# Performance work log

Measured on AMD Instinct MI355X. Metric: run time of the kernel, lower is better.

The kernel has to match this reference:

```python
import math
import jax, jax.numpy as jnp
import numpy as np

B, S, D, H = 4, 2048, 768, 12
HD = D // H  # 64


def setup_inputs() -> dict:
    key = jax.random.key(0)
    ks = jax.random.split(key, 10)
    sc = 0.02
    return {
        "hidden_states": jax.random.normal(ks[0], (B, S, D), dtype=jnp.float32),
        "attention_mask": jax.random.randint(ks[1], (1, H, S, S), 0, 2).astype(jnp.bool_),
        "q_w": jax.random.normal(ks[2], (D, D), dtype=jnp.float32) * sc,
        "q_b": jax.random.normal(ks[3], (D,), dtype=jnp.float32) * sc,
        "k_w": jax.random.normal(ks[4], (D, D), dtype=jnp.float32) * sc,
        "k_b": jax.random.normal(ks[5], (D,), dtype=jnp.float32) * sc,
        "v_w": jax.random.normal(ks[6], (D, D), dtype=jnp.float32) * sc,
        "v_b": jax.random.normal(ks[7], (D,), dtype=jnp.float32) * sc,
        "out_w": jax.random.normal(ks[8], (D, D), dtype=jnp.float32) * sc,
        "out_b": jax.random.normal(ks[9], (D,), dtype=jnp.float32) * sc,
    }


def _split_heads(x):
    # [B, S, D] -> [B, H, S, HD]
    b, s, _ = x.shape
    return x.reshape(b, s, H, HD).transpose(0, 2, 1, 3)


def reference(hidden_states, attention_mask, q_w, q_b, k_w, k_b, v_w, v_b, out_w, out_b):
    q = _split_heads(hidden_states @ q_w.T + q_b)
    k = _split_heads(hidden_states @ k_w.T + k_b)
    v = _split_heads(hidden_states @ v_w.T + v_b)
    scores = jnp.einsum("bhqd,bhkd->bhqk", q, k) / math.sqrt(HD)
    # prune_mode, before softmax: masked_fill(~mask, -inf)
    scores = jnp.where(attention_mask, scores, -jnp.inf)
    probs = jax.nn.softmax(scores, axis=-1)  # [B, H, S, S]
    ctx = jnp.einsum("bhqk,bhkd->bhqd", probs, v)
    ctx = ctx.transpose(0, 2, 1, 3).reshape(hidden_states.shape[0], -1, D)
    return ctx @ out_w.T + out_b
```

## Files before the change

### kernel.cpp

```cpp
#include <hip/hip_runtime.h>
#include <hip/hip_bf16.h>

#define B_ 4
#define S_ 2048
#define D_ 768
#define H_ 12
#define HD_ 64

typedef __attribute__((ext_vector_type(8))) short bf16x8;
typedef __attribute__((ext_vector_type(4))) float floatx4;

#define QSCALE 0.18033688011112042f

__device__ __forceinline__ unsigned short f2bf(float x) {
    union { float f; unsigned int u; } v; v.f = x;
    unsigned int r = v.u + 0x7fffu + ((v.u >> 16) & 1u);
    return (unsigned short)(r >> 16);
}

__device__ __forceinline__ unsigned int pk2bf(float a, float b) {
    __hip_bfloat162 h = __float22bfloat162_rn(make_float2(a, b));
    unsigned int u;
    __builtin_memcpy(&u, &h, 4);
    return u;
}

__device__ __forceinline__ void gload_lds16(const void* g, void* l) {
    __builtin_amdgcn_global_load_lds(
        (const __attribute__((address_space(1))) unsigned int*)g,
        (__attribute__((address_space(3))) unsigned int*)l, 16, 0, 0);
}

__device__ __forceinline__ bf16x8 ld_b64x2(const unsigned short* p) {
    union { bf16x8 v; unsigned long long q[2]; } u;
    u.q[0] = *(const unsigned long long*)p;
    u.q[1] = *(const unsigned long long*)(p + 4);
    return u.v;
}

__global__ void prep(const float* __restrict__ hs,
                     const float* __restrict__ w0, const float* __restrict__ w1,
                     const float* __restrict__ w2, const float* __restrict__ w3,
                     const int* __restrict__ mask,
                     unsigned short* __restrict__ Xb,
                     unsigned short* __restrict__ Wb,
                     unsigned long long* __restrict__ bits) {
    int bid = blockIdx.x;
    int t = threadIdx.x;
    if (bid < 6144) {
        int i = bid * 256 + t;
        float4 f = ((const float4*)hs)[i];
        ushort4 o;
        o.x = f2bf(f.x); o.y = f2bf(f.y); o.z = f2bf(f.z); o.w = f2bf(f.w);
        ((ushort4*)Xb)[i] = o;
    } else if (bid < 8448) {
        int q = bid - 6144;
        int wid = q / 576;
        const float* src = (wid == 0) ? w0 : (wid == 1) ? w1 : (wid == 2) ? w2 : w3;
        unsigned short* d = Wb + (size_t)wid * 589824;
        int i = (q - wid * 576) * 256 + t;
        float4 f = ((const float4*)src)[i];
        ushort4 o;
        o.x = f2bf(f.x); o.y = f2bf(f.y); o.z = f2bf(f.z); o.w = f2bf(f.w);
        ((ushort4*)d)[i] = o;
    } else {
        size_t gw = ((size_t)(bid - 8448) * 256 + t) >> 6;
        int lane = t & 63;
        size_t base = gw * 256;
        unsigned long long b0 = __ballot(mask[base + lane] != 0);
        unsigned long long b1 = __ballot(mask[base + 64 + lane] != 0);
        unsigned long long b2 = __ballot(mask[base + 128 + lane] != 0);
        unsigned long long b3 = __ballot(mask[base + 192 + lane] != 0);
        if (lane == 0) {
            bits[gw * 4 + 0] = b0; bits[gw * 4 + 1] = b1;
            bits[gw * 4 + 2] = b2; bits[gw * 4 + 3] = b3;
        }
    }
}

__global__ __launch_bounds__(256) void qkv_gemm(
    const unsigned short* __restrict__ Xb,
    const unsigned short* __restrict__ Wq, const unsigned short* __restrict__ Wk,
    const unsigned short* __restrict__ Wv,
    const float* __restrict__ bq, const float* __restrict__ bk,
    const float* __restrict__ bv,
    unsigned short* __restrict__ Qo, unsigned short* __restrict__ Ko,
    unsigned short* __restrict__ Vo)
{
    const int z = blockIdx.z;
    const unsigned short* W = (z == 0) ? Wq : (z == 1) ? Wk : Wv;
    const float* bias = (z == 0) ? bq : (z == 1) ? bk : bv;
    unsigned short* Out = (z == 0) ? Qo : (z == 1) ? Ko : Vo;
    const float scale = (z == 0) ? QSCALE : 1.0f;

    const int m0 = blockIdx.x * 128;
    const int n0 = blockIdx.y * 128;

    __shared__ alignas(16) unsigned short SMall[16384];
    unsigned short* SM = SMall;

    const int t = threadIdx.x;
    const int lane = t & 63, w = t >> 6;
    const int c = lane & 15, quad = lane >> 4;
    const int wm = (w & 1) * 64, wn = (w >> 1) * 64;

    const int srowq = lane >> 2, sc8 = (lane & 3) * 8;

    floatx4 acc[4][4];
#pragma unroll
    for (int i = 0; i < 4; i++)
#pragma unroll
        for (int j = 0; j < 4; j++) acc[i][j] = (floatx4){0.f, 0.f, 0.f, 0.f};

#pragma unroll
    for (int i = 0; i < 2; i++) {
        int chunk = i * 4 + w;
        int row = chunk * 16 + srowq;
        gload_lds16(&Xb[(size_t)(m0 + row) * 768 + sc8], &SMall[chunk * 512]);
        gload_lds16(&W [(size_t)(n0 + row) * 768 + sc8], &SMall[4096 + chunk * 512]);
    }

    for (int it = 0; it < 24; it++) {
        const int cur = it & 1;
        __syncthreads();
        if (it + 1 < 24) {
            int k1 = (it + 1) * 32;
#pragma unroll
            for (int i = 0; i < 2; i++) {
                int chunk = i * 4 + w;
                int row = chunk * 16 + srowq;
                gload_lds16(&Xb[(size_t)(m0 + row) * 768 + k1 + sc8],
                            &SMall[(cur ^ 1) * 8192 + chunk * 512]);
                gload_lds16(&W [(size_t)(n0 + row) * 768 + k1 + sc8],
                            &SMall[(cur ^ 1) * 8192 + 4096 + chunk * 512]);
            }
        }
        const unsigned short* As = &SMall[cur * 8192];
        const unsigned short* Bs = As + 4096;
        bf16x8 a[4], b[4];
#pragma unroll
        for (int i = 0; i < 4; i++)
            a[i] = *(const bf16x8*)&As[(wm + i * 16 + c) * 32 + quad * 8];
#pragma unroll
        for (int j = 0; j < 4; j++)
            b[j] = *(const bf16x8*)&Bs[(wn + j * 16 + c) * 32 + quad * 8];
#pragma unroll
        for (int i = 0; i < 4; i++)
#pragma unroll
            for (int j = 0; j < 4; j++)
                acc[i][j] = __builtin_amdgcn_mfma_f32_16x16x32_bf16(
                    a[i], b[j], acc[i][j], 0, 0, 0);
    }
    __syncthreads();

    const int bb = m0 >> 11, ssb = m0 & 2047;
    if (z == 2) {
#pragma unroll
        for (int half = 0; half < 2; half++) {
            if ((w >> 1) == half) {
#pragma unroll
                for (int j = 0; j < 4; j++) {
                    int n_l = j * 16 + c;
                    float bias_n = bias[n0 + half * 64 + n_l];
#pragma unroll
                    for (int i = 0; i < 4; i++) {
#pragma unroll
                        for (int r = 0; r < 4; r++) {
                            int m = wm + i * 16 + quad * 4 + r;
                            int ms = m ^ (c << 3);
                            SM[n_l * 128 + ms] = f2bf(acc[i][j][r] + bias_n);
                        }
                    }
                }
            }
            __syncthreads();
#pragma unroll
            for (int rb = 0; rb < 2; rb++) {
                int n_l = (t >> 3) + rb * 32;
                int ch = t & 7;
                int n_abs = n0 + half * 64 + n_l;
                int hh = n_abs >> 6, dd = n_abs & 63;
                unsigned short* dst =
                    Out + (((size_t)(bb * H_ + hh)) * 64 + dd) * S_ + ssb;
#pragma unroll
                for (int p = 0; p < 2; p++) {
                    int mc = ch + p * 8;
                    uint4 v = *(const uint4*)&SM[n_l * 128 + ((mc ^ (n_l & 15)) * 8)];
                    *(uint4*)&dst[mc * 8] = v;
                }
            }
            __syncthreads();
        }
    } else {
#pragma unroll
        for (int half = 0; half < 2; half++) {
            if ((w >> 1) == half) {
#pragma unroll
                for (int j = 0; j < 4; j++) {
                    float bias_n = bias[n0 + half * 64 + j * 16 + c];
#pragma unroll
                    for (int i = 0; i < 4; i++) {
#pragma unroll
                        for (int r = 0; r < 4; r++) {
                            int m = wm + i * 16 + quad * 4 + r;
                            int chunk = (j * 2 + (c >> 3)) ^ ((m >> 1) & 7);
                            SM[m * 64 + chunk * 8 + (c & 7)] =
                                f2bf((acc[i][j][r] + bias_n) * scale);
                        }
                    }
                }
            }
            __syncthreads();
            {
                int hh = (n0 >> 6) + half;
                unsigned short* dst =
                    Out + ((size_t)(bb * H_ + hh) * S_ + ssb) * 64;
#pragma unroll
                for (int i = 0; i < 4; i++) {
                    int idx = i * 256 + t;
                    int m = idx >> 3, ch = idx & 7;
                    uint4 v = *(const uint4*)&SM[m * 64 + ((ch ^ ((m >> 1) & 7)) * 8)];
                    *(uint4*)&dst[(size_t)m * 64 + ch * 8] = v;
                }
            }
            __syncthreads();
        }
    }
}

__global__ __launch_bounds__(256) void out_gemm(
    const unsigned short* __restrict__ Cb, const unsigned short* __restrict__ Wo,
    const float* __restrict__ bo, float* __restrict__ out)
{
    const int m0 = blockIdx.x * 64;
    const int n0 = blockIdx.y * 128;

    __shared__ alignas(16) unsigned short SMall[12288];

    const int t = threadIdx.x;
    const int lane = t & 63, w = t >> 6;
    const int c = lane & 15, quad = lane >> 4;
    const int wm = (w & 1) * 32, wn = (w >> 1) * 64;

    const int arow = w * 16 + (lane >> 2);
    const int brow0 = (lane >> 2);
    const int sc8 = (lane & 3) * 8;

    floatx4 acc[2][4];
#pragma unroll
    for (int i = 0; i < 2; i++)
#pragma unroll
        for (int j = 0; j < 4; j++) acc[i][j] = (floatx4){0.f, 0.f, 0.f, 0.f};

    gload_lds16(&Cb[(size_t)(m0 + arow) * 768 + sc8], &SMall[w * 512]);
#pragma unroll
    for (int i = 0; i < 2; i++) {
        int chunk = i * 4 + w;
        gload_lds16(&Wo[(size_t)(n0 + chunk * 16 + brow0) * 768 + sc8],
                    &SMall[2048 + chunk * 512]);
    }

    for (int it = 0; it < 24; it++) {
        const int cur = it & 1;
        __syncthreads();
        if (it + 1 < 24) {
            int k1 = (it + 1) * 32;
            gload_lds16(&Cb[(size_t)(m0 + arow) * 768 + k1 + sc8],
                        &SMall[(cur ^ 1) * 6144 + w * 512]);
#pragma unroll
            for (int i = 0; i < 2; i++) {
                int chunk = i * 4 + w;
                gload_lds16(&Wo[(size_t)(n0 + chunk * 16 + brow0) * 768 + k1 + sc8],
                            &SMall[(cur ^ 1) * 6144 + 2048 + chunk * 512]);
            }
        }
        const unsigned short* As = &SMall[cur * 6144];
        const unsigned short* Bs = As + 2048;
        bf16x8 a[2], b[4];
#pragma unroll
        for (int i = 0; i < 2; i++)
            a[i] = *(const bf16x8*)&As[(wm + i * 16 + c) * 32 + quad * 8];
#pragma unroll
        for (int j = 0; j < 4; j++)
            b[j] = *(const bf16x8*)&Bs[(wn + j * 16 + c) * 32 + quad * 8];
#pragma unroll
        for (int i = 0; i < 2; i++)
#pragma unroll
            for (int j = 0; j < 4; j++)
                acc[i][j] = __builtin_amdgcn_mfma_f32_16x16x32_bf16(
                    a[i], b[j], acc[i][j], 0, 0, 0);
    }
    __syncthreads();

    float* SMf = (float*)SMall;
#pragma unroll
    for (int qtr = 0; qtr < 4; qtr++) {
        if ((w >> 1) == (qtr >> 1)) {
#pragma unroll
            for (int jj = 0; jj < 2; jj++) {
                int j = (qtr & 1) * 2 + jj;
                float bias_n = bo[n0 + wn + j * 16 + c];
                int chunk = jj * 4 + (c >> 2);
#pragma unroll
                for (int i = 0; i < 2; i++) {
#pragma unroll
                    for (int r = 0; r < 4; r++) {
                        int m = wm + i * 16 + quad * 4 + r;
                        SMf[m * 32 + ((chunk ^ (m & 7)) * 4) + (c & 3)] =
                            acc[i][j][r] + bias_n;
                    }
                }
            }
        }
        __syncthreads();
#pragma unroll
        for (int i = 0; i < 2; i++) {
            int idx = i * 256 + t;
            int m = idx >> 3, ch = idx & 7;
            float4 v = *(const float4*)&SMf[m * 32 + ((ch ^ (m & 7)) * 4)];
            *(float4*)&out[(size_t)(m0 + m) * 768 + n0 + qtr * 32 + ch * 4] = v;
        }
        __syncthreads();
    }
}

__global__ __launch_bounds__(256) void attn(
    const unsigned short* __restrict__ Q, const unsigned short* __restrict__ K,
    const unsigned short* __restrict__ Vt,
    const unsigned long long* __restrict__ mbits,
    unsigned short* __restrict__ ctx)
{
    const int qt = blockIdx.x;
    const int bh = blockIdx.y;
    const int b = bh / H_, h = bh % H_;

    const unsigned short* Qp = Q + (size_t)bh * S_ * 64 + (size_t)qt * 128 * 64;
    const unsigned short* Kp = K + (size_t)bh * S_ * 64;
    const unsigned short* Vp = Vt + (size_t)bh * 64 * S_;

    __shared__ alignas(16) unsigned short Ks[2][64 * 64];
    __shared__ alignas(16) unsigned short Vs[2][64 * 64];
    __shared__ alignas(16) unsigned short Ps[4][2][16 * 68];

    const int t = threadIdx.x;
    const int lane = t & 63, w = t >> 6;
    const int c = lane & 15, quad = lane >> 4;

    bf16x8 aq[2][2];
#pragma unroll
    for (int st = 0; st < 2; st++) {
        aq[st][0] = *(const bf16x8*)&Qp[(size_t)(w * 32 + st * 16 + c) * 64 + quad * 8];
        aq[st][1] = *(const bf16x8*)&Qp[(size_t)(w * 32 + st * 16 + c) * 64 + 32 + quad * 8];
    }

    const unsigned long long* mrow =
        mbits + ((size_t)h * S_ + qt * 128 + w * 32 + quad * 4) * (S_ / 64);

    floatx4 acc_o[2][4];
#pragma unroll
    for (int st = 0; st < 2; st++)
#pragma unroll
        for (int i = 0; i < 4; i++) acc_o[st][i] = (floatx4){0.f, 0.f, 0.f, 0.f};
    float lp[2][4] = {{0.f, 0.f, 0.f, 0.f}, {0.f, 0.f, 0.f, 0.f}};

    const int srow = (lane >> 3);
    const int rc0 = ((quad     ) ^ (c & 7)) * 8;
    const int rc1 = ((quad + 4) ^ (c & 7)) * 8;

#pragma unroll
    for (int i = 0; i < 2; i++) {
        int chunk = i * 4 + w;
        int row = chunk * 8 + srow;
        int col8 = (((lane & 7) ^ ((row >> 2) & 7))) * 8;
        gload_lds16(&Kp[(size_t)row * 64 + col8], &Ks[0][chunk * 512]);
        gload_lds16(&Vp[(size_t)row * S_ + col8], &Vs[0][chunk * 512]);
    }

    for (int kt = 0; kt < S_ / 64; kt++) {
        const int cur = kt & 1;
        __syncthreads();
        if (kt + 1 < S_ / 64) {
#pragma unroll
            for (int i = 0; i < 2; i++) {
                int chunk = i * 4 + w;
                int row = chunk * 8 + srow;
                int col8 = (((lane & 7) ^ ((row >> 2) & 7))) * 8;
                gload_lds16(&Kp[(size_t)((kt + 1) * 64 + row) * 64 + col8],
                            &Ks[cur ^ 1][chunk * 512]);
                gload_lds16(&Vp[(size_t)row * S_ + (kt + 1) * 64 + col8],
                            &Vs[cur ^ 1][chunk * 512]);
            }
        }

        floatx4 sacc[2][4];
        __builtin_amdgcn_s_setprio(1);
#pragma unroll
        for (int nt = 0; nt < 4; nt++) {
            int kr = 4 * c + nt;
            bf16x8 bk0 = *(const bf16x8*)&Ks[cur][kr * 64 + rc0];
            bf16x8 bk1 = *(const bf16x8*)&Ks[cur][kr * 64 + rc1];
#pragma unroll
            for (int st = 0; st < 2; st++) {
                floatx4 zz = (floatx4){0.f, 0.f, 0.f, 0.f};
                zz = __builtin_amdgcn_mfma_f32_16x16x32_bf16(aq[st][0], bk0, zz, 0, 0, 0);
                zz = __builtin_amdgcn_mfma_f32_16x16x32_bf16(aq[st][1], bk1, zz, 0, 0, 0);
                sacc[st][nt] = zz;
            }
        }
        __builtin_amdgcn_s_setprio(0);

        asm volatile("" ::: "memory");
#pragma unroll
        for (int st = 0; st < 2; st++) {
#pragma unroll
            for (int r = 0; r < 4; r++) {
                unsigned int nib =
                    (unsigned int)(mrow[st * 16 * (S_ / 64) + r * (S_ / 64) + kt] >> (4 * c)) & 15u;
                float p0 = (nib & 1u) ? __builtin_amdgcn_exp2f(sacc[st][0][r]) : 0.f;
                float p1 = (nib & 2u) ? __builtin_amdgcn_exp2f(sacc[st][1][r]) : 0.f;
                float p2 = (nib & 4u) ? __builtin_amdgcn_exp2f(sacc[st][2][r]) : 0.f;
                float p3 = (nib & 8u) ? __builtin_amdgcn_exp2f(sacc[st][3][r]) : 0.f;
                lp[st][r] += (p0 + p1) + (p2 + p3);
                unsigned long long pk =
                    (unsigned long long)pk2bf(p0, p1) |
                    ((unsigned long long)pk2bf(p2, p3) << 32);
                *(unsigned long long*)&Ps[w][st][(quad * 4 + r) * 68 + 4 * c] = pk;
            }
        }
        asm volatile("" ::: "memory");

        bf16x8 ap[2][2];
#pragma unroll
        for (int st = 0; st < 2; st++) {
            ap[st][0] = ld_b64x2(&Ps[w][st][c * 68 + quad * 8]);
            ap[st][1] = ld_b64x2(&Ps[w][st][c * 68 + 32 + quad * 8]);
        }

        __builtin_amdgcn_s_setprio(1);
#pragma unroll
        for (int nt = 0; nt < 4; nt++) {
            int vr = 4 * c + nt;
            bf16x8 bv0 = *(const bf16x8*)&Vs[cur][vr * 64 + rc0];
            bf16x8 bv1 = *(const bf16x8*)&Vs[cur][vr * 64 + rc1];
#pragma unroll
            for (int st = 0; st < 2; st++) {
                acc_o[st][nt] = __builtin_amdgcn_mfma_f32_16x16x32_bf16(ap[st][0], bv0, acc_o[st][nt], 0, 0, 0);
                acc_o[st][nt] = __builtin_amdgcn_mfma_f32_16x16x32_bf16(ap[st][1], bv1, acc_o[st][nt], 0, 0, 0);
            }
        }
        __builtin_amdgcn_s_setprio(0);
    }

#pragma unroll
    for (int st = 0; st < 2; st++)
#pragma unroll
        for (int r = 0; r < 4; r++) {
            float s = lp[st][r];
#pragma unroll
            for (int o = 1; o < 16; o <<= 1) s += __shfl_xor(s, o, 64);
            lp[st][r] = s;
        }

#pragma unroll
    for (int st = 0; st < 2; st++)
#pragma unroll
        for (int nt = 0; nt < 4; nt++)
#pragma unroll
            for (int r = 0; r < 4; r++) {
                int qrow = qt * 128 + w * 32 + st * 16 + quad * 4 + r;
                int dd = 4 * c + nt;
                float v = acc_o[st][nt][r] / lp[st][r];
                ctx[((size_t)b * S_ + qrow) * 768 + h * 64 + dd] = f2bf(v);
            }
}

extern "C" void kernel_launch(void* const* d_in, const int* in_sizes, int n_in,
                              void* d_out, int out_size, void* d_ws, size_t ws_size,
                              hipStream_t stream) {
    const float* hs    = (const float*)d_in[0];
    const int*   mask  = (const int*)d_in[1];
    const float* q_w   = (const float*)d_in[2];
    const float* q_b   = (const float*)d_in[3];
    const float* k_w   = (const float*)d_in[4];
    const float* k_b   = (const float*)d_in[5];
    const float* v_w   = (const float*)d_in[6];
    const float* v_b   = (const float*)d_in[7];
    const float* out_w = (const float*)d_in[8];
    const float* out_b = (const float*)d_in[9];
    float* out = (float*)d_out;

    unsigned short* Xb  = (unsigned short*)d_ws;
    unsigned short* Wqb = Xb + 6291456;
    unsigned short* Wkb = Wqb + 589824;
    unsigned short* Wvb = Wkb + 589824;
    unsigned short* Wob = Wvb + 589824;
    unsigned short* Qb  = Wob + 589824;
    unsigned short* Kb  = Qb + 6291456;
    unsigned short* Vtb = Kb + 6291456;
    unsigned short* Cb  = Vtb + 6291456;
    unsigned long long* mbits = (unsigned long long*)(Cb + 6291456);

    prep<<<57600, 256, 0, stream>>>(hs, q_w, k_w, v_w, out_w, mask, Xb, Wqb, mbits);
    qkv_gemm<<<dim3(64, 6, 3), 256, 0, stream>>>(Xb, Wqb, Wkb, Wvb,
                                                 q_b, k_b, v_b, Qb, Kb, Vtb);
    attn<<<dim3(16, 48), 256, 0, stream>>>(Qb, Kb, Vtb, mbits, Cb);
    out_gemm<<<dim3(128, 6), 256, 0, stream>>>(Cb, Wob, out_b, out);
}
```

Before: 497.0 us.

## Coarsen mask-pack blocks, remap block order per XCD, split QK softmax into halves

The mask-packing part of prep now has each block handle eight wave-groups instead of one, which cuts the prep grid from 57600 to 14592 blocks. The qkv_gemm, out_gemm and attn kernels remap their linear block IDs with an interleave of 8, so that neighbouring tiles that share operands land on the same XCD and its L2. The attention inner loop is split into two halves, so the exp/mask/pack work of one half can overlap with the MFMAs of the other, and the s_setprio hints are removed. These changes are meant to lower launch and scheduling overhead, improve cache locality, and hide softmax latency behind matrix ops, at the cost of smaller 4-byte LDS stores and a different instruction schedule.

```diff
diff --git a/kernel.cpp b/kernel.cpp
--- a/kernel.cpp
+++ b/kernel.cpp
@@ -64,16 +64,20 @@
         o.x = f2bf(f.x); o.y = f2bf(f.y); o.z = f2bf(f.z); o.w = f2bf(f.w);
         ((ushort4*)d)[i] = o;
     } else {
-        size_t gw = ((size_t)(bid - 8448) * 256 + t) >> 6;
-        int lane = t & 63;
-        size_t base = gw * 256;
-        unsigned long long b0 = __ballot(mask[base + lane] != 0);
-        unsigned long long b1 = __ballot(mask[base + 64 + lane] != 0);
-        unsigned long long b2 = __ballot(mask[base + 128 + lane] != 0);
-        unsigned long long b3 = __ballot(mask[base + 192 + lane] != 0);
-        if (lane == 0) {
-            bits[gw * 4 + 0] = b0; bits[gw * 4 + 1] = b1;
-            bits[gw * 4 + 2] = b2; bits[gw * 4 + 3] = b3;
+        int q = bid - 8448;
+        int lane = t & 63, wv = t >> 6;
+#pragma unroll
+        for (int j = 0; j < 8; j++) {
+            size_t gw = (size_t)q * 32 + j * 4 + wv;
+            size_t base = gw * 256;
+            unsigned long long b0 = __ballot(mask[base + lane] != 0);
+            unsigned long long b1 = __ballot(mask[base + 64 + lane] != 0);
+            unsigned long long b2 = __ballot(mask[base + 128 + lane] != 0);
+            unsigned long long b3 = __ballot(mask[base + 192 + lane] != 0);
+            if (lane == 0) {
+                bits[gw * 4 + 0] = b0; bits[gw * 4 + 1] = b1;
+                bits[gw * 4 + 2] = b2; bits[gw * 4 + 3] = b3;
+            }
         }
     }
 }
@@ -87,14 +91,17 @@
     unsigned short* __restrict__ Qo, unsigned short* __restrict__ Ko,
     unsigned short* __restrict__ Vo)
 {
-    const int z = blockIdx.z;
+    const int lin = blockIdx.x + 64 * (blockIdx.y + 6 * blockIdx.z);
+    const int nn = (lin & 7) * 144 + (lin >> 3);
+    const int z = nn % 3;
+    const int xy = nn / 3;
+    const int m0 = (xy & 63) * 128;
+    const int n0 = (xy >> 6) * 128;
+
     const unsigned short* W = (z == 0) ? Wq : (z == 1) ? Wk : Wv;
     const float* bias = (z == 0) ? bq : (z == 1) ? bk : bv;
     unsigned short* Out = (z == 0) ? Qo : (z == 1) ? Ko : Vo;
     const float scale = (z == 0) ? QSCALE : 1.0f;
-
-    const int m0 = blockIdx.x * 128;
-    const int n0 = blockIdx.y * 128;
 
     __shared__ alignas(16) unsigned short SMall[16384];
     unsigned short* SM = SMall;
@@ -232,8 +239,10 @@
     const unsigned short* __restrict__ Cb, const unsigned short* __restrict__ Wo,
     const float* __restrict__ bo, float* __restrict__ out)
 {
-    const int m0 = blockIdx.x * 64;
-    const int n0 = blockIdx.y * 128;
+    const int lin = blockIdx.x + 128 * blockIdx.y;
+    const int nn = (lin & 7) * 96 + (lin >> 3);
+    const int m0 = (nn & 127) * 64;
+    const int n0 = (nn >> 7) * 128;
 
     __shared__ alignas(16) unsigned short SMall[12288];
 
@@ -330,8 +339,10 @@
     const unsigned long long* __restrict__ mbits,
     unsigned short* __restrict__ ctx)
 {
-    const int qt = blockIdx.x;
-    const int bh = blockIdx.y;
+    const int lin = blockIdx.y * 16 + blockIdx.x;
+    const int nn = (lin & 7) * 96 + (lin >> 3);
+    const int qt = nn & 15;
+    const int bh = nn >> 4;
     const int b = bh / H_, h = bh % H_;
 
     const unsigned short* Qp = Q + (size_t)bh * S_ * 64 + (size_t)qt * 128 * 64;
@@ -392,42 +403,41 @@
             }
         }
 
-        floatx4 sacc[2][4];
-        __builtin_amdgcn_s_setprio(1);
-#pragma unroll
-        for (int nt = 0; nt < 4; nt++) {
-            int kr = 4 * c + nt;
-            bf16x8 bk0 = *(const bf16x8*)&Ks[cur][kr * 64 + rc0];
-            bf16x8 bk1 = *(const bf16x8*)&Ks[cur][kr * 64 + rc1];
+#pragma unroll
+        for (int p = 0; p < 2; p++) {
+            floatx4 zz[2][2];
+            zz[0][0] = (floatx4){0.f, 0.f, 0.f, 0.f};
+            zz[0][1] = (floatx4){0.f, 0.f, 0.f, 0.f};
+            zz[1][0] = (floatx4){0.f, 0.f, 0.f, 0.f};
+            zz[1][1] = (floatx4){0.f, 0.f, 0.f, 0.f};
+#pragma unroll
+            for (int q2 = 0; q2 < 2; q2++) {
+                int kr = 4 * c + 2 * p + q2;
+                bf16x8 bk0 = *(const bf16x8*)&Ks[cur][kr * 64 + rc0];
+                bf16x8 bk1 = *(const bf16x8*)&Ks[cur][kr * 64 + rc1];
+                zz[0][q2] = __builtin_amdgcn_mfma_f32_16x16x32_bf16(aq[0][0], bk0, zz[0][q2], 0, 0, 0);
+                zz[0][q2] = __builtin_amdgcn_mfma_f32_16x16x32_bf16(aq[0][1], bk1, zz[0][q2], 0, 0, 0);
+                zz[1][q2] = __builtin_amdgcn_mfma_f32_16x16x32_bf16(aq[1][0], bk0, zz[1][q2], 0, 0, 0);
+                zz[1][q2] = __builtin_amdgcn_mfma_f32_16x16x32_bf16(aq[1][1], bk1, zz[1][q2], 0, 0, 0);
+            }
+
+            asm volatile("" ::: "memory");
 #pragma unroll
             for (int st = 0; st < 2; st++) {
-                floatx4 zz = (floatx4){0.f, 0.f, 0.f, 0.f};
-                zz = __builtin_amdgcn_mfma_f32_16x16x32_bf16(aq[st][0], bk0, zz, 0, 0, 0);
-                zz = __builtin_amdgcn_mfma_f32_16x16x32_bf16(aq[st][1], bk1, zz, 0, 0, 0);
-                sacc[st][nt] = zz;
-            }
-        }
-        __builtin_amdgcn_s_setprio(0);
-
-        asm volatile("" ::: "memory");
-#pragma unroll
-        for (int st = 0; st < 2; st++) {
-#pragma unroll
-            for (int r = 0; r < 4; r++) {
-                unsigned int nib =
-                    (unsigned int)(mrow[st * 16 * (S_ / 64) + r * (S_ / 64) + kt] >> (4 * c)) & 15u;
-                float p0 = (nib & 1u) ? __builtin_amdgcn_exp2f(sacc[st][0][r]) : 0.f;
-                float p1 = (nib & 2u) ? __builtin_amdgcn_exp2f(sacc[st][1][r]) : 0.f;
-                float p2 = (nib & 4u) ? __builtin_amdgcn_exp2f(sacc[st][2][r]) : 0.f;
-                float p3 = (nib & 8u) ? __builtin_amdgcn_exp2f(sacc[st][3][r]) : 0.f;
-                lp[st][r] += (p0 + p1) + (p2 + p3);
-                unsigned long long pk =
-                    (unsigned long long)pk2bf(p0, p1) |
-                    ((unsigned long long)pk2bf(p2, p3) << 32);
-                *(unsigned long long*)&Ps[w][st][(quad * 4 + r) * 68 + 4 * c] = pk;
-            }
-        }
-        asm volatile("" ::: "memory");
+#pragma unroll
+                for (int r = 0; r < 4; r++) {
+                    unsigned int n2 =
+                        (unsigned int)(mrow[st * 16 * (S_ / 64) + r * (S_ / 64) + kt]
+                                       >> (4 * c + 2 * p)) & 3u;
+                    float p0 = (n2 & 1u) ? __builtin_amdgcn_exp2f(zz[st][0][r]) : 0.f;
+                    float p1 = (n2 & 2u) ? __builtin_amdgcn_exp2f(zz[st][1][r]) : 0.f;
+                    lp[st][r] += p0 + p1;
+                    *(unsigned int*)&Ps[w][st][(quad * 4 + r) * 68 + 4 * c + 2 * p] =
+                        pk2bf(p0, p1);
+                }
+            }
+            asm volatile("" ::: "memory");
+        }
 
         bf16x8 ap[2][2];
 #pragma unroll
@@ -436,7 +446,6 @@
             ap[st][1] = ld_b64x2(&Ps[w][st][c * 68 + 32 + quad * 8]);
         }
 
-        __builtin_amdgcn_s_setprio(1);
 #pragma unroll
         for (int nt = 0; nt < 4; nt++) {
             int vr = 4 * c + nt;
@@ -448,7 +457,6 @@
                 acc_o[st][nt] = __builtin_amdgcn_mfma_f32_16x16x32_bf16(ap[st][1], bv1, acc_o[st][nt], 0, 0, 0);
             }
         }
-        __builtin_amdgcn_s_setprio(0);
     }
 
 #pragma unroll
@@ -500,7 +508,7 @@
     unsigned short* Cb  = Vtb + 6291456;
     unsigned long long* mbits = (unsigned long long*)(Cb + 6291456);
 
-    prep<<<57600, 256, 0, stream>>>(hs, q_w, k_w, v_w, out_w, mask, Xb, Wqb, mbits);
+    prep<<<14592, 256, 0, stream>>>(hs, q_w, k_w, v_w, out_w, mask, Xb, Wqb, mbits);
     qkv_gemm<<<dim3(64, 6, 3), 256, 0, stream>>>(Xb, Wqb, Wkb, Wvb,
                                                  q_b, k_b, v_b, Qb, Kb, Vtb);
     attn<<<dim3(16, 48), 256, 0, stream>>>(Qb, Kb, Vtb, mbits, Cb);
```

After: 500.3 us. About the same (+0.7%).
